# Kernel tuning notes

Measured on AMD Instinct MI355X. Metric: run time of the kernel, lower is better.

Reference implementation:

```python
import jax, jax.numpy as jnp
import numpy as np

DIM, HEADS, DHEAD, CTX_DIM = 1024, 16, 64, 768
INNER = HEADS * DHEAD  # 1024
FF_HID = 4 * DIM       # 4096
EPS = 1e-5


def _ln(x, g, b):
    mu = jnp.mean(x, axis=-1, keepdims=True)
    var = jnp.mean(jnp.square(x - mu), axis=-1, keepdims=True)
    return (x - mu) * jax.lax.rsqrt(var + EPS) * g + b


def _attn(x, ctx, Wq, Wk, Wv, Wo, bo):
    b, n, _ = x.shape
    m = ctx.shape[1]
    q = (x @ Wq).reshape(b, n, HEADS, DHEAD)
    k = (ctx @ Wk).reshape(b, m, HEADS, DHEAD)
    v = (ctx @ Wv).reshape(b, m, HEADS, DHEAD)
    scale = DHEAD ** -0.5
    sim = jnp.einsum('bihd,bjhd->bhij', q, k) * scale
    attn = jax.nn.softmax(sim, axis=-1)
    out = jnp.einsum('bhij,bjhd->bihd', attn, v).reshape(b, n, INNER)
    return out @ Wo + bo


def setup_inputs() -> dict:
    key = jax.random.key(0)
    ks = jax.random.split(key, 24)
    def w(k, shape, fan_in):
        return jax.random.normal(k, shape, jnp.float32) * (fan_in ** -0.5)
    inp = {
        'x': jax.random.normal(ks[0], (2, 2048, DIM), jnp.float32),
        'context': jax.random.normal(ks[1], (2, 77, CTX_DIM), jnp.float32),
        # attn1 (self)
        'Wq1': w(ks[2], (DIM, INNER), DIM), 'Wk1': w(ks[3], (DIM, INNER), DIM),
        'Wv1': w(ks[4], (DIM, INNER), DIM), 'Wo1': w(ks[5], (INNER, DIM), INNER),
        'bo1': jnp.zeros((DIM,), jnp.float32),
        # attn2 (cross)
        'Wq2': w(ks[6], (DIM, INNER), DIM), 'Wk2': w(ks[7], (CTX_DIM, INNER), CTX_DIM),
        'Wv2': w(ks[8], (CTX_DIM, INNER), CTX_DIM), 'Wo2': w(ks[9], (INNER, DIM), INNER),
        'bo2': jnp.zeros((DIM,), jnp.float32),
        # GEGLU FFN
        'Wp': w(ks[10], (DIM, 2 * FF_HID), DIM), 'bp': jnp.zeros((2 * FF_HID,), jnp.float32),
        'W2': w(ks[11], (FF_HID, DIM), FF_HID), 'b2': jnp.zeros((DIM,), jnp.float32),
        # LayerNorms
        'g1': jnp.ones((DIM,), jnp.float32), 'be1': jnp.zeros((DIM,), jnp.float32),
        'g2': jnp.ones((DIM,), jnp.float32), 'be2': jnp.zeros((DIM,), jnp.float32),
        'g3': jnp.ones((DIM,), jnp.float32), 'be3': jnp.zeros((DIM,), jnp.float32),
    }
    return inp


def reference(x, context, Wq1, Wk1, Wv1, Wo1, bo1, Wq2, Wk2, Wv2, Wo2, bo2,
              Wp, bp, W2, b2, g1, be1, g2, be2, g3, be3):
    h = _ln(x, g1, be1)
    x = _attn(h, h, Wq1, Wk1, Wv1, Wo1, bo1) + x
    h = _ln(x, g2, be2)
    x = _attn(h, context, Wq2, Wk2, Wv2, Wo2, bo2) + x
    h = _ln(x, g3, be3)
    y = h @ Wp + bp
    a, gate = y[..., :FF_HID], y[..., FF_HID:]
    x = (a * jax.nn.gelu(gate, approximate=False)) @ W2 + b2 + x
    return x
```

## Files before the change

kernel.cpp:

```cpp
#include <hip/hip_runtime.h>
#include <hip/hip_bf16.h>
#include <math.h>

#define DIMN   1024
#define HEADS  16
#define DHEAD  64
#define CTXD   768
#define FFH    4096
#define NTOK   4096
#define SEQ    2048
#define NCTX   77
#define CTOK   154

typedef unsigned short u16;
typedef __bf16 bf16x8 __attribute__((ext_vector_type(8)));
typedef float  f32x4  __attribute__((ext_vector_type(4)));

__device__ __forceinline__ u16 f2bf(float f) {
  union { float f; unsigned u; } c; c.f = f;
  unsigned r = c.u + 0x7FFFu + ((c.u >> 16) & 1u);
  return (u16)(r >> 16);
}
__device__ __forceinline__ float bf2f(u16 h) {
  union { unsigned u; float f; } c; c.u = ((unsigned)h) << 16; return c.f;
}

__device__ __forceinline__ void gload16(const void* g, void* l) {
  __builtin_amdgcn_global_load_lds(
      (__attribute__((address_space(1))) void*)(void*)(g),
      (__attribute__((address_space(3))) void*)(l), 16, 0, 0);
}

__device__ __forceinline__ f32x4 mfma16(bf16x8 a, bf16x8 b, f32x4 c) {
  return __builtin_amdgcn_mfma_f32_16x16x32_bf16(a, b, c, 0, 0, 0);
}

struct WBatch { const float* s[6]; u16* d[6]; };

template<int NB>
__global__ __launch_bounds__(256)
void wconvB_k(WBatch wb, int K, int N)
{
  __shared__ u16 t[64][65];
  const float* __restrict__ W  = wb.s[blockIdx.z];
  u16* __restrict__       WT   = wb.d[blockIdx.z];
  int n0 = blockIdx.x * 64, k0 = blockIdx.y * 64;
  int tid = threadIdx.x;
  int rr = tid >> 4, cc = tid & 15;
#pragma unroll
  for (int i = 0; i < 4; ++i) {
    int kr = rr + i * 16;
    const float4 v = *(const float4*)&W[(size_t)(k0 + kr) * N + n0 + cc * 4];
    t[kr][cc*4+0] = f2bf(v.x); t[kr][cc*4+1] = f2bf(v.y);
    t[kr][cc*4+2] = f2bf(v.z); t[kr][cc*4+3] = f2bf(v.w);
  }
  __syncthreads();
#pragma unroll
  for (int i = 0; i < 4; ++i) {
    int nr = rr + i * 16;
    int r0 = cc * 4;
    ushort4 o;
    o.x = t[r0+0][nr]; o.y = t[r0+1][nr]; o.z = t[r0+2][nr]; o.w = t[r0+3][nr];
    *(ushort4*)&WT[(size_t)(n0 + nr) * K + k0 + r0] = o;
  }
}

__global__ __launch_bounds__(256)
void wconv_k(const float* __restrict__ W, u16* __restrict__ WT, int K, int N)
{
  __shared__ u16 t[64][65];
  int n0 = blockIdx.x * 64, k0 = blockIdx.y * 64;
  int tid = threadIdx.x;
  int rr = tid >> 4, cc = tid & 15;
#pragma unroll
  for (int i = 0; i < 4; ++i) {
    int kr = rr + i * 16;
    const float4 v = *(const float4*)&W[(size_t)(k0 + kr) * N + n0 + cc * 4];
    t[kr][cc*4+0] = f2bf(v.x); t[kr][cc*4+1] = f2bf(v.y);
    t[kr][cc*4+2] = f2bf(v.z); t[kr][cc*4+3] = f2bf(v.w);
  }
  __syncthreads();
#pragma unroll
  for (int i = 0; i < 4; ++i) {
    int nr = rr + i * 16;
    int r0 = cc * 4;
    ushort4 o;
    o.x = t[r0+0][nr]; o.y = t[r0+1][nr]; o.z = t[r0+2][nr]; o.w = t[r0+3][nr];
    *(ushort4*)&WT[(size_t)(n0 + nr) * K + k0 + r0] = o;
  }
}

__global__ void cconv_k(const float* __restrict__ c, u16* __restrict__ o, int n)
{
  int i = blockIdx.x * 256 + threadIdx.x;
  if (i < n) o[i] = f2bf(c[i]);
}

__global__ __launch_bounds__(256)
void ln_k(const float* __restrict__ x, const float* __restrict__ gm,
          const float* __restrict__ bt, u16* __restrict__ o)
{
  int row = blockIdx.x;
  int tid = threadIdx.x;
  const float4 v = *(const float4*)&x[(size_t)row * DIMN + tid * 4];
  float s = v.x + v.y + v.z + v.w;
  float q = v.x*v.x + v.y*v.y + v.z*v.z + v.w*v.w;
#pragma unroll
  for (int off = 32; off; off >>= 1) { s += __shfl_xor(s, off); q += __shfl_xor(q, off); }
  __shared__ float ss[4], qq[4];
  int wave = tid >> 6;
  if ((tid & 63) == 0) { ss[wave] = s; qq[wave] = q; }
  __syncthreads();
  s = ss[0] + ss[1] + ss[2] + ss[3];
  q = qq[0] + qq[1] + qq[2] + qq[3];
  float mu = s * (1.0f / DIMN);
  float var = q * (1.0f / DIMN) - mu * mu;
  float rs = rsqrtf(var + 1e-5f);
  const float4 gv = *(const float4*)&gm[tid * 4];
  const float4 bv = *(const float4*)&bt[tid * 4];
  ushort4 r;
  r.x = f2bf((v.x - mu) * rs * gv.x + bv.x);
  r.y = f2bf((v.y - mu) * rs * gv.y + bv.y);
  r.z = f2bf((v.z - mu) * rs * gv.z + bv.z);
  r.w = f2bf((v.w - mu) * rs * gv.w + bv.w);
  *(ushort4*)&o[(size_t)row * DIMN + tid * 4] = r;
}

template<int MODE>
__global__ __launch_bounds__(512, 4)
void gemm_k(const u16* __restrict__ A, const u16* __restrict__ Bt,
            int M, int N, int K,
            const float* __restrict__ bias, const float* __restrict__ resid,
            u16* __restrict__ obf, float* __restrict__ of32,
            int seq, int vstride,
            u16* __restrict__ ob2, u16* __restrict__ ob3)
{
  __shared__ __align__(16) u16 As[2][128 * 32];
  __shared__ __align__(16) u16 Bs[2][128 * 32];
  const int tid = threadIdx.x;
  const int lane = tid & 63, wave = tid >> 6;
  const int wr = wave >> 1, wc = wave & 1;
  const int g = lane >> 4, r16 = lane & 15;
  const int m0 = blockIdx.x * 128, n0 = blockIdx.y * 128;

  f32x4 acc[2][4] = {};

  const int srow = tid >> 2;
  const int sch  = tid & 3;
  const int schs = sch ^ ((srow >> 1) & 3);
  const int arow = (m0 + srow > M - 1) ? (M - 1) : (m0 + srow);
  const size_t abase = (size_t)arow * K + schs * 8;
  const size_t bbase = (size_t)(n0 + srow) * K + schs * 8;

  auto stage = [&](int buf, int kt) {
    gload16(A  + abase + kt, &As[buf][tid * 8]);
    gload16(Bt + bbase + kt, &Bs[buf][tid * 8]);
  };

  stage(0, 0);

  const int nkt = K >> 5;
  for (int t = 0; t < nkt; ++t) {
    const int cur = t & 1;
    if (t + 1 < nkt) {
      stage(cur ^ 1, (t + 1) << 5);
      asm volatile("s_waitcnt vmcnt(2)" ::: "memory");
    } else {
      asm volatile("s_waitcnt vmcnt(0)" ::: "memory");
    }
    __builtin_amdgcn_s_barrier();

    bf16x8 af[2], bfr[4];
#pragma unroll
    for (int mi = 0; mi < 2; ++mi) {
      int r = wr * 32 + mi * 16 + r16;
      int cph = g ^ ((r >> 1) & 3);
      af[mi] = *(const bf16x8*)&As[cur][(r * 4 + cph) * 8];
    }
#pragma unroll
    for (int ni = 0; ni < 4; ++ni) {
      int r = wc * 64 + ni * 16 + r16;
      int cph = g ^ ((r >> 1) & 3);
      bfr[ni] = *(const bf16x8*)&Bs[cur][(r * 4 + cph) * 8];
    }
    __builtin_amdgcn_s_setprio(1);
#pragma unroll
    for (int mi = 0; mi < 2; ++mi)
#pragma unroll
      for (int ni = 0; ni < 4; ++ni)
        acc[mi][ni] = mfma16(af[mi], bfr[ni], acc[mi][ni]);
    __builtin_amdgcn_s_setprio(0);

    __builtin_amdgcn_s_barrier();
  }

  const int grp = n0 >> 10;
#pragma unroll
  for (int ni = 0; ni < 4; ++ni) {
    int col = n0 + wc * 64 + ni * 16 + r16;
    float bv = 0.0f;
    if constexpr (MODE == 0 || MODE == 2) bv = bias ? bias[col] : 0.0f;
    const int c1 = col & 1023;
#pragma unroll
    for (int mi = 0; mi < 2; ++mi) {
      f32x4 c = acc[mi][ni];
#pragma unroll
      for (int rg = 0; rg < 4; ++rg) {
        int row = m0 + wr * 32 + mi * 16 + g * 4 + rg;
        if (row < M) {
          float v = c[rg] + bv;
          if constexpr (MODE == 0) {
            obf[(size_t)row * N + col] = f2bf(v);
          } else if constexpr (MODE == 2) {
            size_t o = (size_t)row * N + col;
            of32[o] = v + resid[o];
          } else if constexpr (MODE == 3) {
            int b = row / seq, srow_ = row - b * seq;
            int jg = srow_ >> 6, j = srow_ & 63;
            int pos = jg * 64 + ((j & 15) << 2) + (j >> 4);
            obf[((size_t)b * HEADS * DHEAD + c1) * vstride + pos] = f2bf(v);
          } else if constexpr (MODE == 4) {
            if (grp == 0) {
              obf[(size_t)row * 1024 + c1] = f2bf(v);
            } else if (grp == 1) {
              ob2[(size_t)row * 1024 + c1] = f2bf(v);
            } else {
              int b = row / seq, srow_ = row - b * seq;
              int jg = srow_ >> 6, j = srow_ & 63;
              int pos = jg * 64 + ((j & 15) << 2) + (j >> 4);
              ob3[((size_t)b * HEADS * DHEAD + c1) * vstride + pos] = f2bf(v);
            }
          } else {
            if (grp == 0) {
              obf[(size_t)row * 1024 + c1] = f2bf(v);
            } else {
              int b = row / seq, srow_ = row - b * seq;
              int jg = srow_ >> 6, j = srow_ & 63;
              int pos = jg * 64 + ((j & 15) << 2) + (j >> 4);
              ob3[((size_t)b * HEADS * DHEAD + c1) * vstride + pos] = f2bf(v);
            }
          }
        }
      }
    }
  }
}

template<int MODE>
__global__ __launch_bounds__(512, 2)
void gemm64_k(const u16* __restrict__ A, const u16* __restrict__ Bt,
              int M, int N, int K,
              const float* __restrict__ bias, const float* __restrict__ resid,
              u16* __restrict__ obf, float* __restrict__ of32)
{
  __shared__ __align__(16) u16 As[2][128 * 64];
  __shared__ __align__(16) u16 Bs[2][128 * 64];
  const int tid = threadIdx.x;
  const int lane = tid & 63, wave = tid >> 6;
  const int wr = wave >> 1, wc = wave & 1;
  const int g = lane >> 4, r16 = lane & 15;
  const int m0 = blockIdx.x * 128, n0 = blockIdx.y * 128;

  f32x4 acc[2][4] = {};

  int aro[2], bro[2], scs[2];
#pragma unroll
  for (int i = 0; i < 2; ++i) {
    const int c = tid + i * 512;
    const int r = c >> 3, ch = c & 7;
    scs[i] = ch ^ (r & 7);
    aro[i] = (m0 + r > M - 1) ? (M - 1) : (m0 + r);
    bro[i] = n0 + r;
  }

  auto stage = [&](int buf, int kt) {
#pragma unroll
    for (int i = 0; i < 2; ++i) {
      const int c = tid + i * 512;
      gload16(A  + (size_t)aro[i] * K + kt + scs[i] * 8, &As[buf][c * 8]);
      gload16(Bt + (size_t)bro[i] * K + kt + scs[i] * 8, &Bs[buf][c * 8]);
    }
  };

  stage(0, 0);

  const int nkt = K >> 6;
  for (int t = 0; t < nkt; ++t) {
    const int cur = t & 1;
    if (t + 1 < nkt) {
      stage(cur ^ 1, (t + 1) << 6);
      asm volatile("s_waitcnt vmcnt(4)" ::: "memory");
    } else {
      asm volatile("s_waitcnt vmcnt(0)" ::: "memory");
    }
    __builtin_amdgcn_s_barrier();

#pragma unroll
    for (int ks = 0; ks < 2; ++ks) {
      bf16x8 af[2], bfr[4];
#pragma unroll
      for (int mi = 0; mi < 2; ++mi) {
        int r = wr * 32 + mi * 16 + r16;
        int cph = (ks * 4 + g) ^ (r & 7);
        af[mi] = *(const bf16x8*)&As[cur][(r * 8 + cph) * 8];
      }
#pragma unroll
      for (int ni = 0; ni < 4; ++ni) {
        int r = wc * 64 + ni * 16 + r16;
        int cph = (ks * 4 + g) ^ (r & 7);
        bfr[ni] = *(const bf16x8*)&Bs[cur][(r * 8 + cph) * 8];
      }
      __builtin_amdgcn_s_setprio(1);
#pragma unroll
      for (int mi = 0; mi < 2; ++mi)
#pragma unroll
        for (int ni = 0; ni < 4; ++ni)
          acc[mi][ni] = mfma16(af[mi], bfr[ni], acc[mi][ni]);
      __builtin_amdgcn_s_setprio(0);
    }

    __builtin_amdgcn_s_barrier();
  }

#pragma unroll
  for (int ni = 0; ni < 4; ++ni) {
    int col = n0 + wc * 64 + ni * 16 + r16;
    float bv = bias ? bias[col] : 0.0f;
#pragma unroll
    for (int mi = 0; mi < 2; ++mi) {
      f32x4 c = acc[mi][ni];
#pragma unroll
      for (int rg = 0; rg < 4; ++rg) {
        int row = m0 + wr * 32 + mi * 16 + g * 4 + rg;
        if (row < M) {
          float v = c[rg] + bv;
          if constexpr (MODE == 0) {
            obf[(size_t)row * N + col] = f2bf(v);
          } else {
            size_t o = (size_t)row * N + col;
            of32[o] = v + resid[o];
          }
        }
      }
    }
  }
}

__global__ __launch_bounds__(512, 2)
void geglu_k(const u16* __restrict__ A, const u16* __restrict__ B1t,
             const u16* __restrict__ B2t,
             const float* __restrict__ ba, const float* __restrict__ bg,
             u16* __restrict__ out, int M, int N)
{
  __shared__ __align__(16) u16 As[2][128 * 32];
  __shared__ __align__(16) u16 B1s[2][128 * 32];
  __shared__ __align__(16) u16 B2s[2][128 * 32];
  const int tid = threadIdx.x;
  const int lane = tid & 63, wave = tid >> 6;
  const int wr = wave >> 1, wc = wave & 1;
  const int g = lane >> 4, r16 = lane & 15;
  const int m0 = blockIdx.x * 128, n0 = blockIdx.y * 128;
  const int K = 1024;

  f32x4 acca[2][4] = {}, accg[2][4] = {};

  const int srow = tid >> 2;
  const int sch  = tid & 3;
  const int schs = sch ^ ((srow >> 1) & 3);
  const size_t abase = (size_t)(m0 + srow) * K + schs * 8;
  const size_t bbase = (size_t)(n0 + srow) * K + schs * 8;

  auto stage = [&](int buf, int kt) {
    gload16(A   + abase + kt, &As[buf][tid * 8]);
    gload16(B1t + bbase + kt, &B1s[buf][tid * 8]);
    gload16(B2t + bbase + kt, &B2s[buf][tid * 8]);
  };

  stage(0, 0);

  const int nkt = K >> 5;
  for (int t = 0; t < nkt; ++t) {
    const int cur = t & 1;
    if (t + 1 < nkt) {
      stage(cur ^ 1, (t + 1) << 5);
      asm volatile("s_waitcnt vmcnt(3)" ::: "memory");
    } else {
      asm volatile("s_waitcnt vmcnt(0)" ::: "memory");
    }
    __builtin_amdgcn_s_barrier();

    bf16x8 af[2], b1f[4], b2f[4];
#pragma unroll
    for (int mi = 0; mi < 2; ++mi) {
      int r = wr * 32 + mi * 16 + r16;
      int cph = g ^ ((r >> 1) & 3);
      af[mi] = *(const bf16x8*)&As[cur][(r * 4 + cph) * 8];
    }
#pragma unroll
    for (int ni = 0; ni < 4; ++ni) {
      int r = wc * 64 + ni * 16 + r16;
      int cph = g ^ ((r >> 1) & 3);
      b1f[ni] = *(const bf16x8*)&B1s[cur][(r * 4 + cph) * 8];
      b2f[ni] = *(const bf16x8*)&B2s[cur][(r * 4 + cph) * 8];
    }
    __builtin_amdgcn_s_setprio(1);
#pragma unroll
    for (int mi = 0; mi < 2; ++mi)
#pragma unroll
      for (int ni = 0; ni < 4; ++ni) {
        acca[mi][ni] = mfma16(af[mi], b1f[ni], acca[mi][ni]);
        accg[mi][ni] = mfma16(af[mi], b2f[ni], accg[mi][ni]);
      }
    __builtin_amdgcn_s_setprio(0);

    __builtin_amdgcn_s_barrier();
  }

#pragma unroll
  for (int ni = 0; ni < 4; ++ni) {
    int col = n0 + wc * 64 + ni * 16 + r16;
    float bva = ba[col], bvg = bg[col];
#pragma unroll
    for (int mi = 0; mi < 2; ++mi) {
#pragma unroll
      for (int rg = 0; rg < 4; ++rg) {
        int row = m0 + wr * 32 + mi * 16 + g * 4 + rg;
        float a  = acca[mi][ni][rg] + bva;
        float gt = accg[mi][ni][rg] + bvg;
        float gl = 0.5f * gt * (1.0f + erff(gt * 0.70710678f));
        out[(size_t)row * N + col] = f2bf(a * gl);
      }
    }
  }
}

__global__ __launch_bounds__(256)
void attn_k(const u16* __restrict__ q, const u16* __restrict__ k,
            const u16* __restrict__ vt, u16* __restrict__ o,
            int kvlen, int seqk, int vstride)
{
  __shared__ __align__(16) u16 Ks[2][64 * 64];
  __shared__ __align__(16) u16 Vs[2][64 * 64];
  __shared__ __align__(16) u16 Ps[4][32 * 72];
  const int tid = threadIdx.x, lane = tid & 63, wave = tid >> 6;
  const int g = lane >> 4, r16 = lane & 15;
  const int bh = blockIdx.y;
  const int b = bh >> 4, h = bh & 15;
  const int q0 = blockIdx.x * 128 + wave * 32;
  const float C = 0.18033688f;

  bf16x8 aq[2][2];
#pragma unroll
  for (int qs = 0; qs < 2; ++qs) {
    const size_t qoff = (size_t)(b * SEQ + q0 + qs * 16 + r16) * DIMN + h * DHEAD;
#pragma unroll
    for (int kc = 0; kc < 2; ++kc)
      aq[qs][kc] = *(const bf16x8*)&q[qoff + kc * 32 + g * 8];
  }
  asm volatile("" :: "v"(aq[0][0]), "v"(aq[0][1]), "v"(aq[1][0]), "v"(aq[1][1]));

  f32x4 oacc[2][4] = {};
  float mi[2][4], li[2][4];
#pragma unroll
  for (int qs = 0; qs < 2; ++qs)
#pragma unroll
    for (int rg = 0; rg < 4; ++rg) { mi[qs][rg] = -3e38f; li[qs][rg] = 0.f; }

  const size_t vtbase = (size_t)(b * HEADS + h) * DHEAD * vstride;
  const size_t kbase  = (size_t)b * seqk * DIMN + h * DHEAD;
  const int nkv = (kvlen + 63) >> 6;

  auto stage = [&](int buf, int kv0) {
#pragma unroll
    for (int i = 0; i < 2; ++i) {
      const int c = tid + i * 256;
      const int row = c >> 3, ch = c & 7;
      const int chs = ch ^ (row & 7);
      int kr = kv0 + row; if (kr > kvlen - 1) kr = kvlen - 1;
      gload16(k + kbase + (size_t)kr * DIMN + chs * 8, &Ks[buf][c * 8]);
    }
#pragma unroll
    for (int i = 0; i < 2; ++i) {
      const int c = tid + i * 256;
      const int row = c >> 3, ch = c & 7;
      const int chs = ch ^ (row & 7);
      gload16(vt + vtbase + (size_t)row * vstride + kv0 + chs * 8, &Vs[buf][c * 8]);
    }
  };

  stage(0, 0);

  for (int kvb = 0; kvb < nkv; ++kvb) {
    const int kv0 = kvb * 64;
    const int cur = kvb & 1;
    if (kvb + 1 < nkv) {
      stage(cur ^ 1, kv0 + 64);
      asm volatile("s_waitcnt vmcnt(4)" ::: "memory");
    } else {
      asm volatile("s_waitcnt vmcnt(0)" ::: "memory");
    }
    __builtin_amdgcn_s_barrier();

    f32x4 sa[2][4];
#pragma unroll
    for (int qs = 0; qs < 2; ++qs)
#pragma unroll
      for (int st = 0; st < 4; ++st) sa[qs][st] = (f32x4){0.f, 0.f, 0.f, 0.f};
    __builtin_amdgcn_s_setprio(1);
#pragma unroll
    for (int st = 0; st < 4; ++st) {
      const int kvr = st * 16 + r16;
#pragma unroll
      for (int kc = 0; kc < 2; ++kc) {
        const int chs = (kc * 4 + g) ^ (kvr & 7);
        const bf16x8 kf = *(const bf16x8*)&Ks[cur][kvr * 64 + chs * 8];
        sa[0][st] = mfma16(aq[0][kc], kf, sa[0][st]);
        sa[1][st] = mfma16(aq[1][kc], kf, sa[1][st]);
      }
    }
    __builtin_amdgcn_s_setprio(0);

    if (kv0 + 64 > kvlen) {
#pragma unroll
      for (int st = 0; st < 4; ++st)
        if (kv0 + st * 16 + r16 >= kvlen) {
#pragma unroll
          for (int qs = 0; qs < 2; ++qs)
#pragma unroll
            for (int rg = 0; rg < 4; ++rg) sa[qs][st][rg] = -3e38f;
        }
    }

    float bad = 0.f;
    float m4v[2][4];
#pragma unroll
    for (int qs = 0; qs < 2; ++qs)
#pragma unroll
      for (int rg = 0; rg < 4; ++rg) {
        float m4 = fmaxf(fmaxf(sa[qs][0][rg], sa[qs][1][rg]),
                         fmaxf(sa[qs][2][rg], sa[qs][3][rg]));
        m4v[qs][rg] = m4;
        bad = fmaxf(bad, m4 - mi[qs][rg]);
      }
    if (__any(bad > 16.0f)) {
#pragma unroll
      for (int qs = 0; qs < 2; ++qs)
#pragma unroll
        for (int rg = 0; rg < 4; ++rg) {
          float mx = m4v[qs][rg];
#pragma unroll
          for (int off = 1; off < 16; off <<= 1) mx = fmaxf(mx, __shfl_xor(mx, off));
          const float nm = fmaxf(mi[qs][rg], mx);
          const float corr = __builtin_amdgcn_exp2f((mi[qs][rg] - nm) * C);
          mi[qs][rg] = nm;
          li[qs][rg] *= corr;
#pragma unroll
          for (int ds = 0; ds < 4; ++ds) oacc[qs][ds][rg] *= corr;
        }
    }

#pragma unroll
    for (int qs = 0; qs < 2; ++qs) {
#pragma unroll
      for (int rg = 0; rg < 4; ++rg) {
        const float mc = mi[qs][rg] * C;
        const float p0 = __builtin_amdgcn_exp2f(__builtin_fmaf(sa[qs][0][rg], C, -mc));
        const float p1 = __builtin_amdgcn_exp2f(__builtin_fmaf(sa[qs][1][rg], C, -mc));
        const float p2 = __builtin_amdgcn_exp2f(__builtin_fmaf(sa[qs][2][rg], C, -mc));
        const float p3 = __builtin_amdgcn_exp2f(__builtin_fmaf(sa[qs][3][rg], C, -mc));
        li[qs][rg] += (p0 + p1) + (p2 + p3);
        unsigned lo, hi;
        asm("v_cvt_pk_bf16_f32 %0, %1, %2" : "=v"(lo) : "v"(p0), "v"(p1));
        asm("v_cvt_pk_bf16_f32 %0, %1, %2" : "=v"(hi) : "v"(p2), "v"(p3));
        const int prow = qs * 16 + g * 4 + rg;
        uint2 pk; pk.x = lo; pk.y = hi;
        *(uint2*)&Ps[wave][prow * 72 + r16 * 4] = pk;
      }
    }

    __builtin_amdgcn_s_setprio(1);
#pragma unroll
    for (int kc = 0; kc < 2; ++kc) {
      const bf16x8 pa0 = *(const bf16x8*)&Ps[wave][(r16)      * 72 + kc * 32 + g * 8];
      const bf16x8 pa1 = *(const bf16x8*)&Ps[wave][(16 + r16) * 72 + kc * 32 + g * 8];
#pragma unroll
      for (int ds = 0; ds < 4; ++ds) {
        const int dr = ds * 16 + r16;
        const int chs = (kc * 4 + g) ^ (dr & 7);
        const bf16x8 vf = *(const bf16x8*)&Vs[cur][dr * 64 + chs * 8];
        oacc[0][ds] = mfma16(pa0, vf, oacc[0][ds]);
        oacc[1][ds] = mfma16(pa1, vf, oacc[1][ds]);
      }
    }
    __builtin_amdgcn_s_setprio(0);

    __builtin_amdgcn_s_barrier();
  }

#pragma unroll
  for (int qs = 0; qs < 2; ++qs)
#pragma unroll
    for (int rg = 0; rg < 4; ++rg) {
      float s = li[qs][rg];
#pragma unroll
      for (int off = 1; off < 16; off <<= 1) s += __shfl_xor(s, off);
      li[qs][rg] = s;
    }

#pragma unroll
  for (int qs = 0; qs < 2; ++qs)
#pragma unroll
    for (int rg = 0; rg < 4; ++rg) {
      const float inv = 1.0f / li[qs][rg];
      const int row = q0 + qs * 16 + g * 4 + rg;
      const size_t base = (size_t)(b * SEQ + row) * DIMN + h * DHEAD;
#pragma unroll
      for (int ds = 0; ds < 4; ++ds)
        o[base + ds * 16 + r16] = f2bf(oacc[qs][ds][rg] * inv);
    }
}

extern "C" void kernel_launch(void* const* d_in, const int* in_sizes, int n_in,
                              void* d_out, int out_size, void* d_ws, size_t ws_size,
                              hipStream_t stream)
{
  const float* x   = (const float*)d_in[0];
  const float* ctx = (const float*)d_in[1];
  const float* Wq1 = (const float*)d_in[2];
  const float* Wk1 = (const float*)d_in[3];
  const float* Wv1 = (const float*)d_in[4];
  const float* Wo1 = (const float*)d_in[5];
  const float* bo1 = (const float*)d_in[6];
  const float* Wq2 = (const float*)d_in[7];
  const float* Wk2 = (const float*)d_in[8];
  const float* Wv2 = (const float*)d_in[9];
  const float* Wo2 = (const float*)d_in[10];
  const float* bo2 = (const float*)d_in[11];
  const float* Wp  = (const float*)d_in[12];
  const float* bp  = (const float*)d_in[13];
  const float* W2  = (const float*)d_in[14];
  const float* b2  = (const float*)d_in[15];
  const float* g1  = (const float*)d_in[16];
  const float* be1 = (const float*)d_in[17];
  const float* g2  = (const float*)d_in[18];
  const float* be2 = (const float*)d_in[19];
  const float* g3  = (const float*)d_in[20];
  const float* be3 = (const float*)d_in[21];

  char* ws = (char*)d_ws;
  size_t off = 0;
  auto alloc = [&](size_t bytes) -> void* {
    void* p = ws + off;
    off += (bytes + 255) & ~(size_t)255;
    return p;
  };

  u16* WqT1 = (u16*)alloc((size_t)1024 * 1024 * 2);
  u16* WkT1 = (u16*)alloc((size_t)1024 * 1024 * 2);
  u16* WvT1 = (u16*)alloc((size_t)1024 * 1024 * 2);
  u16* WoT1 = (u16*)alloc((size_t)1024 * 1024 * 2);
  u16* WqT2 = (u16*)alloc((size_t)1024 * 1024 * 2);
  u16* WkT2 = (u16*)alloc((size_t)1024 * 768 * 2);
  u16* WvT2 = (u16*)alloc((size_t)1024 * 768 * 2);
  u16* WoT2 = (u16*)alloc((size_t)1024 * 1024 * 2);
  u16* WpT  = (u16*)alloc((size_t)8192 * 1024 * 2);
  u16* W2T  = (u16*)alloc((size_t)1024 * 4096 * 2);
  float* x1f = (float*)alloc((size_t)NTOK * DIMN * 4);
  float* x2f = (float*)alloc((size_t)NTOK * DIMN * 4);
  u16* ctxb = (u16*)alloc((size_t)CTOK * CTXD * 2);
  u16* k2b  = (u16*)alloc((size_t)CTOK * DIMN * 2);
  u16* vt2b = (u16*)alloc((size_t)2 * HEADS * DHEAD * 128 * 2);
  u16* hb   = (u16*)alloc((size_t)NTOK * DIMN * 2);
  u16* qb   = (u16*)alloc((size_t)NTOK * DIMN * 2);
  u16* kb   = (u16*)alloc((size_t)NTOK * DIMN * 2);
  u16* vtb  = (u16*)alloc((size_t)NTOK * DIMN * 2);
  u16* ab   = (u16*)alloc((size_t)NTOK * DIMN * 2);
  u16* ub   = qb;

  dim3 blk(256);
  dim3 blk5(512);

  WBatch wb6;
  wb6.s[0] = Wq1; wb6.d[0] = WqT1;
  wb6.s[1] = Wk1; wb6.d[1] = WkT1;
  wb6.s[2] = Wv1; wb6.d[2] = WvT1;
  wb6.s[3] = Wo1; wb6.d[3] = WoT1;
  wb6.s[4] = Wq2; wb6.d[4] = WqT2;
  wb6.s[5] = Wo2; wb6.d[5] = WoT2;
  wconvB_k<6><<<dim3(16, 16, 6), blk, 0, stream>>>(wb6, 1024, 1024);
  WBatch wb2;
  wb2.s[0] = Wk2; wb2.d[0] = WkT2;
  wb2.s[1] = Wv2; wb2.d[1] = WvT2;
  wb2.s[2] = nullptr; wb2.d[2] = nullptr;
  wb2.s[3] = nullptr; wb2.d[3] = nullptr;
  wb2.s[4] = nullptr; wb2.d[4] = nullptr;
  wb2.s[5] = nullptr; wb2.d[5] = nullptr;
  wconvB_k<2><<<dim3(16, 12, 2), blk, 0, stream>>>(wb2, 768, 1024);
  wconv_k<<<dim3(128, 16), blk, 0, stream>>>(Wp, WpT, 1024, 8192);
  wconv_k<<<dim3(16, 64), blk, 0, stream>>>(W2, W2T, 4096, 1024);
  cconv_k<<<dim3((CTOK * CTXD + 255) / 256), blk, 0, stream>>>(ctx, ctxb, CTOK * CTXD);

  ln_k<<<NTOK, 256, 0, stream>>>(x, g1, be1, hb);
  gemm_k<4><<<dim3(32, 24), blk5, 0, stream>>>(hb, WqT1, NTOK, 3072, 1024, nullptr, nullptr, qb, nullptr, SEQ, SEQ, kb, vtb);
  attn_k<<<dim3(16, 32), blk, 0, stream>>>(qb, kb, vtb, ab, SEQ, SEQ, SEQ);
  gemm64_k<2><<<dim3(32, 8), blk5, 0, stream>>>(ab, WoT1, NTOK, 1024, 1024, bo1, x, nullptr, x1f);

  ln_k<<<NTOK, 256, 0, stream>>>(x1f, g2, be2, hb);
  gemm64_k<0><<<dim3(32, 8), blk5, 0, stream>>>(hb, WqT2, NTOK, 1024, 1024, nullptr, nullptr, qb, nullptr);
  gemm_k<5><<<dim3(2, 16), blk5, 0, stream>>>(ctxb, WkT2, CTOK, 2048, 768, nullptr, nullptr, k2b, nullptr, NCTX, 128, nullptr, vt2b);
  attn_k<<<dim3(16, 32), blk, 0, stream>>>(qb, k2b, vt2b, ab, NCTX, NCTX, 128);
  gemm64_k<2><<<dim3(32, 8), blk5, 0, stream>>>(ab, WoT2, NTOK, 1024, 1024, bo2, x1f, nullptr, x2f);

  ln_k<<<NTOK, 256, 0, stream>>>(x2f, g3, be3, hb);
  geglu_k<<<dim3(32, 32), blk5, 0, stream>>>(hb, WpT, WpT + (size_t)4096 * 1024, bp, bp + 4096, ub, NTOK, FFH);
  gemm64_k<2><<<dim3(32, 8), blk5, 0, stream>>>(ub, W2T, NTOK, 1024, 4096, b2, x2f, nullptr, (float*)d_out);

  (void)in_sizes; (void)n_in; (void)out_size; (void)ws_size;
}
```

Before: 404.6 us.

## Store residual stream in bf16 and remap attention block order

The intermediate residual activations x1 and x2 are now stored as bf16 instead of fp32. New GEMM epilogue modes read and write bf16 residuals, and a bf16-input LayerNorm kernel replaces the fp32 one, which roughly halves residual memory traffic. The attention kernel also remaps its block index so that consecutive blocks spread across heads, which may change cache or scheduling behaviour. This costs precision in the residual path, because rounding error accumulates in bf16 before the final output.

New measurement: 401.0 us. About the same (-0.9%).

```diff
diff --git a/kernel.cpp b/kernel.cpp
--- a/kernel.cpp
+++ b/kernel.cpp
@@ -126,6 +126,38 @@
   *(ushort4*)&o[(size_t)row * DIMN + tid * 4] = r;
 }
 
+__global__ __launch_bounds__(256)
+void ln_b_k(const u16* __restrict__ x, const float* __restrict__ gm,
+            const float* __restrict__ bt, u16* __restrict__ o)
+{
+  int row = blockIdx.x;
+  int tid = threadIdx.x;
+  const ushort4 u = *(const ushort4*)&x[(size_t)row * DIMN + tid * 4];
+  float4 v;
+  v.x = bf2f(u.x); v.y = bf2f(u.y); v.z = bf2f(u.z); v.w = bf2f(u.w);
+  float s = v.x + v.y + v.z + v.w;
+  float q = v.x*v.x + v.y*v.y + v.z*v.z + v.w*v.w;
+#pragma unroll
+  for (int off = 32; off; off >>= 1) { s += __shfl_xor(s, off); q += __shfl_xor(q, off); }
+  __shared__ float ss[4], qq[4];
+  int wave = tid >> 6;
+  if ((tid & 63) == 0) { ss[wave] = s; qq[wave] = q; }
+  __syncthreads();
+  s = ss[0] + ss[1] + ss[2] + ss[3];
+  q = qq[0] + qq[1] + qq[2] + qq[3];
+  float mu = s * (1.0f / DIMN);
+  float var = q * (1.0f / DIMN) - mu * mu;
+  float rs = rsqrtf(var + 1e-5f);
+  const float4 gv = *(const float4*)&gm[tid * 4];
+  const float4 bv = *(const float4*)&bt[tid * 4];
+  ushort4 r;
+  r.x = f2bf((v.x - mu) * rs * gv.x + bv.x);
+  r.y = f2bf((v.y - mu) * rs * gv.y + bv.y);
+  r.z = f2bf((v.z - mu) * rs * gv.z + bv.z);
+  r.w = f2bf((v.w - mu) * rs * gv.w + bv.w);
+  *(ushort4*)&o[(size_t)row * DIMN + tid * 4] = r;
+}
+
 template<int MODE>
 __global__ __launch_bounds__(512, 4)
 void gemm_k(const u16* __restrict__ A, const u16* __restrict__ Bt,
@@ -199,7 +231,7 @@
   for (int ni = 0; ni < 4; ++ni) {
     int col = n0 + wc * 64 + ni * 16 + r16;
     float bv = 0.0f;
-    if constexpr (MODE == 0 || MODE == 2) bv = bias ? bias[col] : 0.0f;
+    if constexpr (MODE == 0) bv = bias ? bias[col] : 0.0f;
     const int c1 = col & 1023;
 #pragma unroll
     for (int mi = 0; mi < 2; ++mi) {
@@ -211,14 +243,6 @@
           float v = c[rg] + bv;
           if constexpr (MODE == 0) {
             obf[(size_t)row * N + col] = f2bf(v);
-          } else if constexpr (MODE == 2) {
-            size_t o = (size_t)row * N + col;
-            of32[o] = v + resid[o];
-          } else if constexpr (MODE == 3) {
-            int b = row / seq, srow_ = row - b * seq;
-            int jg = srow_ >> 6, j = srow_ & 63;
-            int pos = jg * 64 + ((j & 15) << 2) + (j >> 4);
-            obf[((size_t)b * HEADS * DHEAD + c1) * vstride + pos] = f2bf(v);
           } else if constexpr (MODE == 4) {
             if (grp == 0) {
               obf[(size_t)row * 1024 + c1] = f2bf(v);
@@ -250,7 +274,8 @@
 __global__ __launch_bounds__(512, 2)
 void gemm64_k(const u16* __restrict__ A, const u16* __restrict__ Bt,
               int M, int N, int K,
-              const float* __restrict__ bias, const float* __restrict__ resid,
+              const float* __restrict__ bias, const float* __restrict__ residf,
+              const u16* __restrict__ residb,
               u16* __restrict__ obf, float* __restrict__ of32)
 {
   __shared__ __align__(16) u16 As[2][128 * 64];
@@ -334,11 +359,15 @@
         int row = m0 + wr * 32 + mi * 16 + g * 4 + rg;
         if (row < M) {
           float v = c[rg] + bv;
+          size_t o = (size_t)row * N + col;
           if constexpr (MODE == 0) {
-            obf[(size_t)row * N + col] = f2bf(v);
+            obf[o] = f2bf(v);
+          } else if constexpr (MODE == 6) {
+            obf[o] = f2bf(v + residf[o]);
+          } else if constexpr (MODE == 7) {
+            obf[o] = f2bf(v + bf2f(residb[o]));
           } else {
-            size_t o = (size_t)row * N + col;
-            of32[o] = v + resid[o];
+            of32[o] = v + bf2f(residb[o]);
           }
         }
       }
@@ -444,9 +473,14 @@
   __shared__ __align__(16) u16 Ps[4][32 * 72];
   const int tid = threadIdx.x, lane = tid & 63, wave = tid >> 6;
   const int g = lane >> 4, r16 = lane & 15;
-  const int bh = blockIdx.y;
+
+  const int L  = blockIdx.y * 16 + blockIdx.x;
+  const int c8 = L & 7, tt = L >> 3;
+  const int bx = tt & 15;
+  const int bh = c8 + 8 * (tt >> 4);
+
   const int b = bh >> 4, h = bh & 15;
-  const int q0 = blockIdx.x * 128 + wave * 32;
+  const int q0 = bx * 128 + wave * 32;
   const float C = 0.18033688f;
 
   bf16x8 aq[2][2];
@@ -665,8 +699,8 @@
   u16* WoT2 = (u16*)alloc((size_t)1024 * 1024 * 2);
   u16* WpT  = (u16*)alloc((size_t)8192 * 1024 * 2);
   u16* W2T  = (u16*)alloc((size_t)1024 * 4096 * 2);
-  float* x1f = (float*)alloc((size_t)NTOK * DIMN * 4);
-  float* x2f = (float*)alloc((size_t)NTOK * DIMN * 4);
+  u16* x1b  = (u16*)alloc((size_t)NTOK * DIMN * 2);
+  u16* x2b  = (u16*)alloc((size_t)NTOK * DIMN * 2);
   u16* ctxb = (u16*)alloc((size_t)CTOK * CTXD * 2);
   u16* k2b  = (u16*)alloc((size_t)CTOK * DIMN * 2);
   u16* vt2b = (u16*)alloc((size_t)2 * HEADS * DHEAD * 128 * 2);
@@ -703,17 +737,17 @@
   ln_k<<<NTOK, 256, 0, stream>>>(x, g1, be1, hb);
   gemm_k<4><<<dim3(32, 24), blk5, 0, stream>>>(hb, WqT1, NTOK, 3072, 1024, nullptr, nullptr, qb, nullptr, SEQ, SEQ, kb, vtb);
   attn_k<<<dim3(16, 32), blk, 0, stream>>>(qb, kb, vtb, ab, SEQ, SEQ, SEQ);
-  gemm64_k<2><<<dim3(32, 8), blk5, 0, stream>>>(ab, WoT1, NTOK, 1024, 1024, bo1, x, nullptr, x1f);
-
-  ln_k<<<NTOK, 256, 0, stream>>>(x1f, g2, be2, hb);
-  gemm64_k<0><<<dim3(32, 8), blk5, 0, stream>>>(hb, WqT2, NTOK, 1024, 1024, nullptr, nullptr, qb, nullptr);
+  gemm64_k<6><<<dim3(32, 8), blk5, 0, stream>>>(ab, WoT1, NTOK, 1024, 1024, bo1, x, nullptr, x1b, nullptr);
+
+  ln_b_k<<<NTOK, 256, 0, stream>>>(x1b, g2, be2, hb);
+  gemm64_k<0><<<dim3(32, 8), blk5, 0, stream>>>(hb, WqT2, NTOK, 1024, 1024, nullptr, nullptr, nullptr, qb, nullptr);
   gemm_k<5><<<dim3(2, 16), blk5, 0, stream>>>(ctxb, WkT2, CTOK, 2048, 768, nullptr, nullptr, k2b, nullptr, NCTX, 128, nullptr, vt2b);
   attn_k<<<dim3(16, 32), blk, 0, stream>>>(qb, k2b, vt2b, ab, NCTX, NCTX, 128);
-  gemm64_k<2><<<dim3(32, 8), blk5, 0, stream>>>(ab, WoT2, NTOK, 1024, 1024, bo2, x1f, nullptr, x2f);
-
-  ln_k<<<NTOK, 256, 0, stream>>>(x2f, g3, be3, hb);
+  gemm64_k<7><<<dim3(32, 8), blk5, 0, stream>>>(ab, WoT2, NTOK, 1024, 1024, bo2, nullptr, x1b, x2b, nullptr);
+
+  ln_b_k<<<NTOK, 256, 0, stream>>>(x2b, g3, be3, hb);
   geglu_k<<<dim3(32, 32), blk5, 0, stream>>>(hb, WpT, WpT + (size_t)4096 * 1024, bp, bp + 4096, ub, NTOK, FFH);
-  gemm64_k<2><<<dim3(32, 8), blk5, 0, stream>>>(ub, W2T, NTOK, 1024, 4096, b2, x2f, nullptr, (float*)d_out);
+  gemm64_k<8><<<dim3(32, 8), blk5, 0, stream>>>(ub, W2T, NTOK, 1024, 4096, b2, nullptr, x2b, nullptr, (float*)d_out);
 
   (void)in_sizes; (void)n_in; (void)out_size; (void)ws_size;
 }
```
